# Kernel tuning notes

Hardware: AMD Instinct MI355X
Metric: run time of the kernel (lower is better)

The kernel has to match this reference:

```python
import jax, jax.numpy as jnp
import numpy as np

N = 768
C = 256  # in_features == out_features (required by Linear(in_features+3, 1))

def _leaky(x):
    return jnp.where(x >= 0, x, 0.2 * x)

def setup_inputs() -> dict:
    key = jax.random.key(0)
    ks = jax.random.split(key, 10)
    features = jax.random.normal(ks[0], (N, C), dtype=jnp.float32)
    coordinates = jax.random.normal(ks[1], (N, 3), dtype=jnp.float32)
    adj = jax.random.uniform(ks[2], (N, N), dtype=jnp.float32)  # unused by forward, kept for signature fidelity
    # Learned params
    FC = jax.random.normal(ks[3], (C, C), dtype=jnp.float32) * (1.414 / jnp.sqrt(C))
    # Conv1d(2,1,kernel=1): weight [out=1, in=2, k=1] -> 2 scalars + bias
    fc_w = jax.random.normal(ks[4], (2,), dtype=jnp.float32) * 0.5
    fc_b = jax.random.normal(ks[5], (1,), dtype=jnp.float32) * 0.1
    sc_w = jax.random.normal(ks[6], (2,), dtype=jnp.float32) * 0.5
    sc_b = jax.random.normal(ks[7], (1,), dtype=jnp.float32) * 0.1
    # Linear(C+3, 1)
    lin_w = jax.random.normal(ks[8], (C + 3,), dtype=jnp.float32) * (1.0 / jnp.sqrt(C + 3))
    lin_b = jax.random.normal(ks[9], (1,), dtype=jnp.float32) * 0.1
    return {"features": features, "coordinates": coordinates, "adj": adj,
            "FC": FC, "fc_w": fc_w, "fc_b": fc_b, "sc_w": sc_w, "sc_b": sc_b,
            "lin_w": lin_w, "lin_b": lin_b}

def reference(features, coordinates, adj, FC, fc_w, fc_b, sc_w, sc_b, lin_w, lin_b):
    n = features.shape[0]
    f_input = features @ FC  # [N, C]
    # torch's repeat(1,N).view + repeat(N,1) builds pairs (i, j); the 1x1 Conv1d over
    # the 2 stacked channels is exactly w0*x_i + w1*x_j + b, then LeakyReLU(0.2).
    f_map = _leaky(fc_w[0] * f_input[:, None, :] + fc_w[1] * f_input[None, :, :] + fc_b[0])  # [N,N,C]
    s_map = _leaky(sc_w[0] * coordinates[:, None, :] + sc_w[1] * coordinates[None, :, :] + sc_b[0])  # [N,N,3]
    # Linear(C+3, 1) on cat([f_map, s_map], -1), then LeakyReLU -> [N, N]
    scores = _leaky(jnp.einsum('ijc,c->ij', f_map, lin_w[:f_input.shape[1]])
                    + jnp.einsum('ijk,k->ij', s_map, lin_w[f_input.shape[1]:])
                    + lin_b[0])
    attention = jax.nn.softmax(scores, axis=1)  # row softmax (dim=1)
    h_prime = attention @ f_input  # [N, C]
    return jax.nn.elu(h_prime)  # concat=True path
```

## Files before the change

kernel.cpp:

```cpp
#include <hip/hip_runtime.h>
#include <math.h>

#define NN 768
#define CC 256
#define TI 3
#define RT 12
#define JC 192
#define NJC 4

__device__ __forceinline__ float leaky(float x) { return x >= 0.0f ? x : 0.2f * x; }

__device__ __forceinline__ float waveMax(float v) {
    #pragma unroll
    for (int o = 32; o > 0; o >>= 1) v = fmaxf(v, __shfl_xor(v, o, 64));
    return v;
}
__device__ __forceinline__ float waveSum(float v) {
    #pragma unroll
    for (int o = 32; o > 0; o >>= 1) v += __shfl_xor(v, o, 64);
    return v;
}

__global__ __launch_bounds__(768) void k_prep(
    const float* __restrict__ features,
    const float* __restrict__ FC,
    const float* __restrict__ fc_w,
    const float* __restrict__ fc_b,
    const float* __restrict__ lin_w,
    float* __restrict__ f,
    float* __restrict__ g,
    float* __restrict__ D0,
    float* __restrict__ D1)
{
    __shared__ float sA[TI * CC];
    __shared__ float sredD[12], sredW[12];

    const int t  = threadIdx.x;
    const int r  = t >> 8;
    const int c  = t & 255;
    const int i0 = blockIdx.x * TI;

    sA[r * CC + c] = features[(i0 + r) * CC + c];
    __syncthreads();

    float a = 0.f;
    const float* fcp = FC + c;
    const float* ap  = sA + r * CC;
    #pragma unroll 8
    for (int k = 0; k < CC; ++k)
        a = fmaf(ap[k], fcp[k * CC], a);

    const float w1 = fc_w[1], b = fc_b[0];
    f[(i0 + r) * CC + c] = a;
    g[c * NN + i0 + r]   = fmaf(w1, a, b);

    const float lw = lin_w[c];
    float dv = waveSum(lw * a);
    float wv = waveSum(lw);
    const int wid = t >> 6;
    if ((t & 63) == 0) { sredD[wid] = dv; sredW[wid] = wv; }
    __syncthreads();
    if (t < TI) {
        float D = sredD[t*4] + sredD[t*4+1] + sredD[t*4+2] + sredD[t*4+3];
        float W = sredW[t*4] + sredW[t*4+1] + sredW[t*4+2] + sredW[t*4+3];
        D0[i0 + t] = fc_w[0] * D;
        D1[i0 + t] = fmaf(w1, D, b * W);
    }
}

__global__ __launch_bounds__(768) void k_attn(
    const float* __restrict__ f,
    const float* __restrict__ g,
    const float* __restrict__ D0,
    const float* __restrict__ D1,
    const float* __restrict__ coords,
    const float* __restrict__ fc_w,
    const float* __restrict__ sc_w,
    const float* __restrict__ sc_b,
    const float* __restrict__ lin_w,
    const float* __restrict__ lin_b,
    float* __restrict__ hp,
    float* __restrict__ Mp,
    float* __restrict__ Lp)
{
    __shared__ float4 su4[4 * CC];
    __shared__ float  pe[RT * JC];
    __shared__ float  sredm[12][3];
    __shared__ float  sreds[12][3];

    const int t  = threadIdx.x;
    const int it = blockIdx.x >> 2;
    const int jc = blockIdx.x & 3;
    const int i0 = it * RT;
    const int jb = jc * JC;
    const int q  = t / JC;
    const int jj = t - q * JC;
    const int j  = jb + jj;
    const int wid  = t >> 6;
    const int lane = t & 63;

    if (t < CC) {
        const float w0  = fc_w[0];
        const float wl4 = 0.4f * lin_w[t];
        #pragma unroll
        for (int qq = 0; qq < 4; ++qq)
            su4[qq * CC + t] = make_float4(w0 * f[(i0 + 3*qq + 0)*CC + t],
                                           w0 * f[(i0 + 3*qq + 1)*CC + t],
                                           w0 * f[(i0 + 3*qq + 2)*CC + t],
                                           wl4);
    }
    __syncthreads();

    float a0 = 0.f, a1 = 0.f, a2 = 0.f;
    const float*  gp  = g + j;
    const float4* sup = su4 + q * CC;
    #pragma unroll 8
    for (int c = 0; c < CC; ++c) {
        float  gj = gp[c * NN];
        float4 u  = sup[c];
        a0 = fmaf(u.w, fabsf(u.x + gj), a0);
        a1 = fmaf(u.w, fabsf(u.y + gj), a1);
        a2 = fmaf(u.w, fabsf(u.z + gj), a2);
    }

    const float sw0 = sc_w[0], sw1 = sc_w[1], sb = sc_b[0], lb = lin_b[0];
    const float lw30 = lin_w[CC], lw31 = lin_w[CC+1], lw32 = lin_w[CC+2];
    const float cj0 = fmaf(sw1, coords[j*3+0], sb);
    const float cj1 = fmaf(sw1, coords[j*3+1], sb);
    const float cj2 = fmaf(sw1, coords[j*3+2], sb);
    const float d1  = D1[j];
    float accs[3] = {a0, a1, a2};
    float scv[3];
    #pragma unroll
    for (int rr = 0; rr < 3; ++rr) {
        const int i = i0 + 3*q + rr;
        float sd = lw30 * leaky(fmaf(sw0, coords[i*3+0], cj0))
                 + lw31 * leaky(fmaf(sw0, coords[i*3+1], cj1))
                 + lw32 * leaky(fmaf(sw0, coords[i*3+2], cj2));
        scv[rr] = leaky(accs[rr] + sd + 0.6f * (D0[i] + d1) + lb);
    }

    #pragma unroll
    for (int rr = 0; rr < 3; ++rr) {
        float v = waveMax(scv[rr]);
        if (lane == 0) sredm[wid][rr] = v;
    }
    __syncthreads();
    float m[3];
    #pragma unroll
    for (int rr = 0; rr < 3; ++rr)
        m[rr] = fmaxf(fmaxf(sredm[3*q][rr], sredm[3*q+1][rr]), sredm[3*q+2][rr]);

    float e[3];
    #pragma unroll
    for (int rr = 0; rr < 3; ++rr) {
        e[rr] = __expf(scv[rr] - m[rr]);
        pe[(3*q + rr) * JC + jj] = e[rr];
        float v = waveSum(e[rr]);
        if (lane == 0) sreds[wid][rr] = v;
    }
    __syncthreads();
    if (jj == 0) {
        #pragma unroll
        for (int rr = 0; rr < 3; ++rr) {
            float l = sreds[3*q][rr] + sreds[3*q+1][rr] + sreds[3*q+2][rr];
            Mp[(i0 + 3*q + rr) * NJC + jc] = m[rr];
            Lp[(i0 + 3*q + rr) * NJC + jc] = l;
        }
    }

    const int rg = t >> 8;
    const int c  = t & 255;
    float h0 = 0.f, h1 = 0.f, h2 = 0.f, h3 = 0.f;
    const float* fp  = f + jb * CC + c;
    const float* pep = pe + (4 * rg) * JC;
    #pragma unroll 4
    for (int jx = 0; jx < JC; ++jx) {
        float fv = fp[jx * CC];
        h0 = fmaf(pep[jx],          fv, h0);
        h1 = fmaf(pep[JC + jx],     fv, h1);
        h2 = fmaf(pep[2*JC + jx],   fv, h2);
        h3 = fmaf(pep[3*JC + jx],   fv, h3);
    }
    float* hpp = hp + ((size_t)jc * NN + i0 + 4*rg) * CC + c;
    hpp[0]      = h0;
    hpp[CC]     = h1;
    hpp[2*CC]   = h2;
    hpp[3*CC]   = h3;
}

__global__ __launch_bounds__(256) void k_comb(
    const float* __restrict__ hp,
    const float* __restrict__ Mp,
    const float* __restrict__ Lp,
    float* __restrict__ out)
{
    const int t = threadIdx.x;
    const int i = blockIdx.x;

    float m0 = Mp[i*NJC+0], m1 = Mp[i*NJC+1], m2 = Mp[i*NJC+2], m3 = Mp[i*NJC+3];
    float M  = fmaxf(fmaxf(m0, m1), fmaxf(m2, m3));
    float w0 = __expf(m0 - M), w1 = __expf(m1 - M);
    float w2 = __expf(m2 - M), w3 = __expf(m3 - M);
    float den = w0*Lp[i*NJC+0] + w1*Lp[i*NJC+1] + w2*Lp[i*NJC+2] + w3*Lp[i*NJC+3];
    float inv = 1.0f / den;

    float num = w0 * hp[((size_t)0*NN + i)*CC + t]
              + w1 * hp[((size_t)1*NN + i)*CC + t]
              + w2 * hp[((size_t)2*NN + i)*CC + t]
              + w3 * hp[((size_t)3*NN + i)*CC + t];
    float v = num * inv;
    out[i*CC + t] = (v > 0.f) ? v : (__expf(v) - 1.0f);
}

extern "C" void kernel_launch(void* const* d_in, const int* in_sizes, int n_in,
                              void* d_out, int out_size, void* d_ws, size_t ws_size,
                              hipStream_t stream) {
    const float* features = (const float*)d_in[0];
    const float* coords   = (const float*)d_in[1];
    const float* FC       = (const float*)d_in[3];
    const float* fc_w     = (const float*)d_in[4];
    const float* fc_b     = (const float*)d_in[5];
    const float* sc_w     = (const float*)d_in[6];
    const float* sc_b     = (const float*)d_in[7];
    const float* lin_w    = (const float*)d_in[8];
    const float* lin_b    = (const float*)d_in[9];
    float* out = (float*)d_out;

    float* f  = (float*)d_ws;
    float* g  = f  + NN*CC;
    float* D0 = g  + CC*NN;
    float* D1 = D0 + NN;
    float* Mp = D1 + NN;
    float* Lp = Mp + NN*NJC;
    float* hp = Lp + NN*NJC;

    k_prep<<<NN/TI, 768, 0, stream>>>(features, FC, fc_w, fc_b, lin_w, f, g, D0, D1);
    k_attn<<<(NN/RT)*NJC, 768, 0, stream>>>(f, g, D0, D1, coords, fc_w, sc_w, sc_b,
                                            lin_w, lin_b, hp, Mp, Lp);
    k_comb<<<NN, 256, 0, stream>>>(hp, Mp, Lp, out);
}
```

Measured before the change: 118.7 us.

## Precompute packed row operands in prep and stage exp weights in global memory

k_prep now writes a packed float4 array holding w0-scaled feature rows plus the scaled lin_w, so k_attn no longer builds this tile in shared memory or waits on a barrier before its main loop. The exponentiated scores are also written to a per-block global scratch in a transposed, padded layout, so the h accumulation loop reads four row weights with one float4 load. Together these drop all large shared-memory arrays from k_attn, which may raise occupancy. In exchange, broadcast reads and the exp round trip now go through the cache hierarchy instead of LDS, adding global traffic and latency. An empty leftover loop remains in the code.

```diff
diff --git a/kernel.cpp b/kernel.cpp
--- a/kernel.cpp
+++ b/kernel.cpp
@@ -7,6 +7,7 @@
 #define RT 12
 #define JC 192
 #define NJC 4
+#define PSTR 16
 
 __device__ __forceinline__ float leaky(float x) { return x >= 0.0f ? x : 0.2f * x; }
 
@@ -30,9 +31,11 @@
     float* __restrict__ f,
     float* __restrict__ g,
     float* __restrict__ D0,
-    float* __restrict__ D1)
+    float* __restrict__ D1,
+    float4* __restrict__ ut4)
 {
     __shared__ float sA[TI * CC];
+    __shared__ float sF[TI * CC];
     __shared__ float sredD[12], sredW[12];
 
     const int t  = threadIdx.x;
@@ -53,6 +56,7 @@
     const float w1 = fc_w[1], b = fc_b[0];
     f[(i0 + r) * CC + c] = a;
     g[c * NN + i0 + r]   = fmaf(w1, a, b);
+    sF[r * CC + c] = a;
 
     const float lw = lin_w[c];
     float dv = waveSum(lw * a);
@@ -66,27 +70,33 @@
         D0[i0 + t] = fc_w[0] * D;
         D1[i0 + t] = fmaf(w1, D, b * W);
     }
+    if (t < CC) {
+        const float w0 = fc_w[0];
+        ut4[blockIdx.x * CC + t] = make_float4(w0 * sF[t],
+                                               w0 * sF[CC + t],
+                                               w0 * sF[2*CC + t],
+                                               0.4f * lin_w[t]);
+    }
 }
 
 __global__ __launch_bounds__(768) void k_attn(
     const float* __restrict__ f,
     const float* __restrict__ g,
+    const float4* __restrict__ ut4,
     const float* __restrict__ D0,
     const float* __restrict__ D1,
     const float* __restrict__ coords,
-    const float* __restrict__ fc_w,
     const float* __restrict__ sc_w,
     const float* __restrict__ sc_b,
     const float* __restrict__ lin_w,
     const float* __restrict__ lin_b,
+    float* __restrict__ pet,
     float* __restrict__ hp,
     float* __restrict__ Mp,
     float* __restrict__ Lp)
 {
-    __shared__ float4 su4[4 * CC];
-    __shared__ float  pe[RT * JC];
-    __shared__ float  sredm[12][3];
-    __shared__ float  sreds[12][3];
+    __shared__ float sredm[12][3];
+    __shared__ float sreds[12][3];
 
     const int t  = threadIdx.x;
     const int it = blockIdx.x >> 2;
@@ -99,25 +109,13 @@
     const int wid  = t >> 6;
     const int lane = t & 63;
 
-    if (t < CC) {
-        const float w0  = fc_w[0];
-        const float wl4 = 0.4f * lin_w[t];
-        #pragma unroll
-        for (int qq = 0; qq < 4; ++qq)
-            su4[qq * CC + t] = make_float4(w0 * f[(i0 + 3*qq + 0)*CC + t],
-                                           w0 * f[(i0 + 3*qq + 1)*CC + t],
-                                           w0 * f[(i0 + 3*qq + 2)*CC + t],
-                                           wl4);
-    }
-    __syncthreads();
-
     float a0 = 0.f, a1 = 0.f, a2 = 0.f;
-    const float*  gp  = g + j;
-    const float4* sup = su4 + q * CC;
+    const float*  gp = g + j;
+    const float4* up = ut4 + (it * 4 + q) * CC;
     #pragma unroll 8
     for (int c = 0; c < CC; ++c) {
         float  gj = gp[c * NN];
-        float4 u  = sup[c];
+        float4 u  = up[c];
         a0 = fmaf(u.w, fabsf(u.x + gj), a0);
         a1 = fmaf(u.w, fabsf(u.y + gj), a1);
         a2 = fmaf(u.w, fabsf(u.z + gj), a2);
@@ -151,13 +149,19 @@
     for (int rr = 0; rr < 3; ++rr)
         m[rr] = fmaxf(fmaxf(sredm[3*q][rr], sredm[3*q+1][rr]), sredm[3*q+2][rr]);
 
+    float* petB = pet + (size_t)blockIdx.x * JC * PSTR;
     float e[3];
     #pragma unroll
     for (int rr = 0; rr < 3; ++rr) {
         e[rr] = __expf(scv[rr] - m[rr]);
-        pe[(3*q + rr) * JC + jj] = e[rr];
+        petB[jj * PSTR + 3*q + rr] = e[rr];
         float v = waveSum(e[rr]);
         if (lane == 0) sreds[wid][rr] = v;
+    }
+    if (jj == 0) {
+        #pragma unroll
+        for (int rr = 0; rr < 3; ++rr) {
+        }
     }
     __syncthreads();
     if (jj == 0) {
@@ -172,21 +176,22 @@
     const int rg = t >> 8;
     const int c  = t & 255;
     float h0 = 0.f, h1 = 0.f, h2 = 0.f, h3 = 0.f;
-    const float* fp  = f + jb * CC + c;
-    const float* pep = pe + (4 * rg) * JC;
+    const float* fp = f + jb * CC + c;
+    const float* pb = petB + 4 * rg;
     #pragma unroll 4
     for (int jx = 0; jx < JC; ++jx) {
-        float fv = fp[jx * CC];
-        h0 = fmaf(pep[jx],          fv, h0);
-        h1 = fmaf(pep[JC + jx],     fv, h1);
-        h2 = fmaf(pep[2*JC + jx],   fv, h2);
-        h3 = fmaf(pep[3*JC + jx],   fv, h3);
+        float  fv = fp[jx * CC];
+        float4 e4 = *(const float4*)(pb + jx * PSTR);
+        h0 = fmaf(e4.x, fv, h0);
+        h1 = fmaf(e4.y, fv, h1);
+        h2 = fmaf(e4.z, fv, h2);
+        h3 = fmaf(e4.w, fv, h3);
     }
     float* hpp = hp + ((size_t)jc * NN + i0 + 4*rg) * CC + c;
-    hpp[0]      = h0;
-    hpp[CC]     = h1;
-    hpp[2*CC]   = h2;
-    hpp[3*CC]   = h3;
+    hpp[0]    = h0;
+    hpp[CC]   = h1;
+    hpp[2*CC] = h2;
+    hpp[3*CC] = h3;
 }
 
 __global__ __launch_bounds__(256) void k_comb(
@@ -227,16 +232,18 @@
     const float* lin_b    = (const float*)d_in[9];
     float* out = (float*)d_out;
 
-    float* f  = (float*)d_ws;
-    float* g  = f  + NN*CC;
-    float* D0 = g  + CC*NN;
-    float* D1 = D0 + NN;
-    float* Mp = D1 + NN;
-    float* Lp = Mp + NN*NJC;
-    float* hp = Lp + NN*NJC;
-
-    k_prep<<<NN/TI, 768, 0, stream>>>(features, FC, fc_w, fc_b, lin_w, f, g, D0, D1);
-    k_attn<<<(NN/RT)*NJC, 768, 0, stream>>>(f, g, D0, D1, coords, fc_w, sc_w, sc_b,
-                                            lin_w, lin_b, hp, Mp, Lp);
+    float* f   = (float*)d_ws;
+    float* g   = f   + NN*CC;
+    float* D0  = g   + CC*NN;
+    float* D1  = D0  + NN;
+    float* Mp  = D1  + NN;
+    float* Lp  = Mp  + NN*NJC;
+    float* hp  = Lp  + NN*NJC;
+    float4* ut4 = (float4*)(hp + (size_t)NJC*NN*CC);
+    float* pet  = (float*)(ut4 + (NN/TI)*CC);
+
+    k_prep<<<NN/TI, 768, 0, stream>>>(features, FC, fc_w, fc_b, lin_w, f, g, D0, D1, ut4);
+    k_attn<<<(NN/RT)*NJC, 768, 0, stream>>>(f, g, ut4, D0, D1, coords, sc_w, sc_b,
+                                            lin_w, lin_b, pet, hp, Mp, Lp);
     k_comb<<<NN, 256, 0, stream>>>(hp, Mp, Lp, out);
 }
```

Result: slower. 148.0 us (+24.7%).
